# Optimization experiments

Measured on AMD Instinct MI355X. Metric: run time of the kernel, lower is better.

Reference implementation:

```python
import jax, jax.numpy as jnp
import numpy as np

NUM_EXPERTS = 8
TOP_K = 2
HIDDEN = 512
INTER = 2048
BALANCE_COEF = 0.01


def setup_inputs() -> dict:
    key = jax.random.key(0)
    ks = jax.random.split(key, 5)
    B, S = 2, 1024
    scale_in = 1.0 / np.sqrt(HIDDEN)
    scale_mid = 1.0 / np.sqrt(INTER)
    return {
        "hidden_states": jax.random.normal(ks[0], (B, S, HIDDEN), jnp.float32),
        "w_router": jax.random.normal(ks[1], (HIDDEN, NUM_EXPERTS), jnp.float32) * scale_in,
        "b_router": jnp.zeros((NUM_EXPERTS,), jnp.float32),
        "w1": jax.random.normal(ks[2], (NUM_EXPERTS, HIDDEN, INTER), jnp.float32) * scale_in,
        "b1": jnp.zeros((NUM_EXPERTS, INTER), jnp.float32),
        "w2": jax.random.normal(ks[3], (NUM_EXPERTS, INTER, HIDDEN), jnp.float32) * scale_mid,
        "b2": jnp.zeros((NUM_EXPERTS, HIDDEN), jnp.float32),
    }


def reference(hidden_states, w_router, b_router, w1, b1, w2, b2):
    B, S, H = hidden_states.shape
    E, K = NUM_EXPERTS, TOP_K

    # ---- Router: softmax over experts, top-k selection, renormalized weights ----
    logits = jnp.einsum("bsh,he->bse", hidden_states, w_router) + b_router  # (B,S,E)
    probs = jax.nn.softmax(logits, axis=-1)
    top_vals, top_idx = jax.lax.top_k(probs, K)                              # (B,S,K)
    routing_weights = top_vals / jnp.sum(top_vals, axis=-1, keepdims=True)   # renorm to sum 1

    # ---- Load-balancing auxiliary loss: coef * E * sum_e f_e * P_e ----
    assign = jax.nn.one_hot(top_idx, E, dtype=probs.dtype)                   # (B,S,K,E)
    f = jnp.mean(assign, axis=(0, 1, 2))                                     # fraction routed per expert
    P = jnp.mean(probs, axis=(0, 1))                                         # mean router prob per expert
    balance_loss = BALANCE_COEF * E * jnp.sum(f * P)

    # ---- Phase 1: flatten (B,S,H) -> (B*S*K, H) token-slots ----
    T = B * S * K
    tokens_flat = jnp.broadcast_to(hidden_states[:, :, None, :], (B, S, K, H)).reshape(T, H)
    weights_flat = routing_weights.reshape(T)
    experts_flat = top_idx.reshape(T)

    # ---- Phase 2: per-expert MLP, masked combine ----
    out_flat = jnp.zeros_like(tokens_flat)
    for e in range(E):
        hmid = jax.nn.gelu(tokens_flat @ w1[e] + b1[e])                      # (T, INTER)
        y = hmid @ w2[e] + b2[e]                                             # (T, H)
        mask = (experts_flat == e)
        out_flat = out_flat + jnp.where(mask[:, None], y * weights_flat[:, None], 0.0)

    # ---- Phase 3: combine over K and residual ----
    combined = out_flat.reshape(B, S, K, H).sum(axis=2)
    output = combined + hidden_states
    return output, balance_loss
```

## Files before the change

kernel.cpp:

```cpp
#include <hip/hip_runtime.h>
#include <math.h>

#define NT 2048
#define TSLOTS 4096
#define HID 512
#define INTER 2048
#define NE 8
#define TM 128
#define BK 32
#define MAXTILES 40
#define PSLOTS 5120

#define WS_HMID      0
#define WS_PROBS     0
#define WS_TOPIDX    65536
#define WS_TOPW      81920
#define WS_TILE_E    20971520
#define WS_TILE_B    20971776
#define WS_TILE_V    20972032
#define WS_PERM      20972288
#define WS_PW        20992768
#define WS_ISLOT     21013248
#define WS_XB        21029632
#define WS_WT        23126784
#define WS_Y         39904000

typedef __attribute__((ext_vector_type(8))) short bf16x8;
typedef __attribute__((ext_vector_type(4))) float f32x4;
typedef __attribute__((ext_vector_type(8))) unsigned short ushort8;

__device__ __forceinline__ unsigned short f2bf(float f) {
    union { float f; unsigned u; } v; v.f = f;
    unsigned r = v.u + 0x7FFF + ((v.u >> 16) & 1);
    return (unsigned short)(r >> 16);
}
__device__ __forceinline__ float bf2f(unsigned short b) {
    union { unsigned u; float f; } v; v.u = ((unsigned)b) << 16;
    return v.f;
}

__device__ __forceinline__ void gload16(const void* g, void* l) {
    __builtin_amdgcn_global_load_lds(
        (const __attribute__((address_space(1))) unsigned int*)g,
        (__attribute__((address_space(3))) unsigned int*)l, 16, 0, 0);
}

__device__ __forceinline__ float gelu_tanh(float x) {
    float x3 = x * x * x;
    return 0.5f * x * (1.0f + tanhf(0.7978845608028654f * (x + 0.044715f * x3)));
}

__global__ __launch_bounds__(64) void route_k(
    const float* __restrict__ hs, const float* __restrict__ wr,
    const float* __restrict__ br,
    unsigned short* __restrict__ xb,
    float* __restrict__ probs, int* __restrict__ topidx, float* __restrict__ topw)
{
    int t = blockIdx.x;
    int lane = threadIdx.x;
    const float* x = hs + (size_t)t * HID + lane * 8;
    float4 v0 = *(const float4*)x;
    float4 v1 = *(const float4*)(x + 4);

    ushort8 ob;
    ob[0] = f2bf(v0.x); ob[1] = f2bf(v0.y); ob[2] = f2bf(v0.z); ob[3] = f2bf(v0.w);
    ob[4] = f2bf(v1.x); ob[5] = f2bf(v1.y); ob[6] = f2bf(v1.z); ob[7] = f2bf(v1.w);
    *(ushort8*)(xb + (size_t)t * HID + lane * 8) = ob;

    float xv[8] = {v0.x, v0.y, v0.z, v0.w, v1.x, v1.y, v1.z, v1.w};
    float acc[NE];
#pragma unroll
    for (int e = 0; e < NE; e++) acc[e] = 0.0f;
    const float* w = wr + (size_t)lane * 8 * NE;
#pragma unroll
    for (int j = 0; j < 8; j++) {
        float4 wa = *(const float4*)(w + j * NE);
        float4 wb = *(const float4*)(w + j * NE + 4);
        acc[0] += xv[j] * wa.x; acc[1] += xv[j] * wa.y;
        acc[2] += xv[j] * wa.z; acc[3] += xv[j] * wa.w;
        acc[4] += xv[j] * wb.x; acc[5] += xv[j] * wb.y;
        acc[6] += xv[j] * wb.z; acc[7] += xv[j] * wb.w;
    }
#pragma unroll
    for (int off = 32; off > 0; off >>= 1) {
#pragma unroll
        for (int e = 0; e < NE; e++) acc[e] += __shfl_down(acc[e], off);
    }
    if (lane == 0) {
        float l[NE], p[NE];
        float m = -1e30f;
#pragma unroll
        for (int e = 0; e < NE; e++) { l[e] = acc[e] + br[e]; m = fmaxf(m, l[e]); }
        float s = 0.0f;
#pragma unroll
        for (int e = 0; e < NE; e++) { p[e] = expf(l[e] - m); s += p[e]; }
        float inv = 1.0f / s;
#pragma unroll
        for (int e = 0; e < NE; e++) { p[e] *= inv; probs[(size_t)t * NE + e] = p[e]; }
        int i1 = 0;
#pragma unroll
        for (int e = 1; e < NE; e++) if (p[e] > p[i1]) i1 = e;
        int i2 = (i1 == 0) ? 1 : 0;
#pragma unroll
        for (int e = 0; e < NE; e++) if (e != i1 && p[e] > p[i2]) i2 = e;
        float denom = 1.0f / (p[i1] + p[i2]);
        topidx[2 * t]     = i1;
        topidx[2 * t + 1] = i2;
        topw[2 * t]       = p[i1] * denom;
        topw[2 * t + 1]   = p[i2] * denom;
    }
}

__global__ __launch_bounds__(256) void plan_k(
    const float* __restrict__ probs, const int* __restrict__ topidx,
    const float* __restrict__ topw,
    int* __restrict__ tile_e, int* __restrict__ tile_b, int* __restrict__ tile_v,
    int* __restrict__ perm, float* __restrict__ pw, int* __restrict__ islot,
    float* __restrict__ loss_out)
{
    int tid = threadIdx.x;
    int lane = tid & 63, wave = tid >> 6;

    float ps[NE];
    int c[NE];
#pragma unroll
    for (int e = 0; e < NE; e++) { ps[e] = 0.0f; c[e] = 0; }
    for (int t = tid; t < NT; t += 256) {
        float4 p0 = *(const float4*)&probs[(size_t)t * NE];
        float4 p1 = *(const float4*)&probs[(size_t)t * NE + 4];
        ps[0] += p0.x; ps[1] += p0.y; ps[2] += p0.z; ps[3] += p0.w;
        ps[4] += p1.x; ps[5] += p1.y; ps[6] += p1.z; ps[7] += p1.w;
    }
    for (int t = tid; t < TSLOTS; t += 256) c[topidx[t]]++;
#pragma unroll
    for (int off = 32; off > 0; off >>= 1) {
#pragma unroll
        for (int e = 0; e < NE; e++) {
            ps[e] += __shfl_down(ps[e], off);
            c[e]  += __shfl_down(c[e], off);
        }
    }
    __shared__ float sps[4][NE];
    __shared__ int sc[4][NE];
    __shared__ int scur[NE];
    if (lane == 0) {
#pragma unroll
        for (int e = 0; e < NE; e++) { sps[wave][e] = ps[e]; sc[wave][e] = c[e]; }
    }
    __syncthreads();
    if (tid == 0) {
        float loss = 0.0f;
        int b = 0, tidx = 0;
        for (int e = 0; e < NE; e++) {
            float pse = sps[0][e] + sps[1][e] + sps[2][e] + sps[3][e];
            int ce = sc[0][e] + sc[1][e] + sc[2][e] + sc[3][e];
            loss += ((float)ce / (float)TSLOTS) * (pse / (float)NT);
            int nt = (ce + TM - 1) / TM;
            scur[e] = b;
            for (int i = 0; i < nt; i++) {
                tile_e[tidx] = e;
                tile_b[tidx] = b + i * TM;
                int v = ce - i * TM;
                tile_v[tidx] = v > TM ? TM : v;
                tidx++;
            }
            b += nt * TM;
        }
        for (; tidx < MAXTILES; tidx++) tile_e[tidx] = -1;
        loss_out[0] = 0.01f * (float)NE * loss;
    }
    __syncthreads();
    for (int t = tid; t < TSLOTS; t += 256) {
        int e = topidx[t];
        int p = atomicAdd(&scur[e], 1);
        perm[p] = t;
        pw[p] = topw[t];
        islot[t] = p;
    }
}

__global__ __launch_bounds__(256) void convT_k(const float* __restrict__ src,
                                               unsigned short* __restrict__ dst,
                                               int K, int N)
{
    int e = blockIdx.z;
    int n0 = blockIdx.x * 32, k0 = blockIdx.y * 32;
    const float* s = src + (size_t)e * K * N;
    unsigned short* d = dst + (size_t)e * N * K;
    __shared__ float T[32][33];
    int tid = threadIdx.x;
    int r = tid >> 3, c4 = (tid & 7) * 4;
    float4 v = *(const float4*)(s + (size_t)(k0 + r) * N + n0 + c4);
    T[r][c4 + 0] = v.x; T[r][c4 + 1] = v.y; T[r][c4 + 2] = v.z; T[r][c4 + 3] = v.w;
    __syncthreads();
    ushort4 o;
    o.x = f2bf(T[c4 + 0][r]); o.y = f2bf(T[c4 + 1][r]);
    o.z = f2bf(T[c4 + 2][r]); o.w = f2bf(T[c4 + 3][r]);
    *(ushort4*)(d + (size_t)(n0 + r) * K + k0 + c4) = o;
}

__global__ __launch_bounds__(256) void gemm1_k(
    const unsigned short* __restrict__ xb, const unsigned short* __restrict__ w1t,
    const float* __restrict__ b1,
    const int* __restrict__ tile_e, const int* __restrict__ tile_b,
    const int* __restrict__ tile_v, const int* __restrict__ perm,
    unsigned short* __restrict__ hmid)
{
    int tt = blockIdx.y;
    int e = tile_e[tt];
    if (e < 0) return;
    int p0 = tile_b[tt], nv = tile_v[tt];
    int n0 = blockIdx.x * 128;

    __shared__ unsigned short As[128 * BK];
    __shared__ unsigned short Bs[128 * BK];

    int tid = threadIdx.x;
    int lane = tid & 63, wave = tid >> 6;
    int wm = (wave >> 1) * 64, wn = (wave & 1) * 64;

    int r1 = tid >> 2, r2 = 64 + r1;
    int kseg = (tid & 3) * 8;
    int tok1 = perm[p0 + ((r1 < nv) ? r1 : 0)] >> 1;
    int tok2 = perm[p0 + ((r2 < nv) ? r2 : 0)] >> 1;
    const unsigned short* a1p = xb + (size_t)tok1 * HID + kseg;
    const unsigned short* a2p = xb + (size_t)tok2 * HID + kseg;
    const unsigned short* bbase = w1t + (size_t)e * INTER * HID;
    const unsigned short* b1p = bbase + (size_t)(n0 + r1) * HID + kseg;
    const unsigned short* b2p = bbase + (size_t)(n0 + r2) * HID + kseg;

    f32x4 acc[4][4] = {};
    int fm = lane & 15, fq = lane >> 4;

    for (int k0 = 0; k0 < HID; k0 += BK) {
        __syncthreads();
        gload16(a1p + k0, (void*)(As + tid * 8));
        gload16(a2p + k0, (void*)(As + 2048 + tid * 8));
        gload16(b1p + k0, (void*)(Bs + tid * 8));
        gload16(b2p + k0, (void*)(Bs + 2048 + tid * 8));
        __syncthreads();
        bf16x8 af[4], bfr[4];
#pragma unroll
        for (int t = 0; t < 4; t++)
            af[t] = *(const bf16x8*)&As[(wm + t * 16 + fm) * BK + fq * 8];
#pragma unroll
        for (int t = 0; t < 4; t++)
            bfr[t] = *(const bf16x8*)&Bs[(wn + t * 16 + fm) * BK + fq * 8];
#pragma unroll
        for (int mt = 0; mt < 4; mt++)
#pragma unroll
            for (int nt = 0; nt < 4; nt++)
                acc[mt][nt] = __builtin_amdgcn_mfma_f32_16x16x32_bf16(
                    af[mt], bfr[nt], acc[mt][nt], 0, 0, 0);
    }

    int cn = lane & 15, crb = (lane >> 4) * 4;
#pragma unroll
    for (int mt = 0; mt < 4; mt++) {
#pragma unroll
        for (int r = 0; r < 4; r++) {
            int m = wm + mt * 16 + crb + r;
            size_t rowoff = (size_t)(p0 + m) * INTER;
#pragma unroll
            for (int nt = 0; nt < 4; nt++) {
                int gn = n0 + wn + nt * 16 + cn;
                float vv = acc[mt][nt][r] + b1[e * INTER + gn];
                hmid[rowoff + gn] = f2bf(gelu_tanh(vv));
            }
        }
    }
}

__global__ __launch_bounds__(256) void gemm2_k(
    const unsigned short* __restrict__ hmid, const unsigned short* __restrict__ w2t,
    const float* __restrict__ b2,
    const int* __restrict__ tile_e, const int* __restrict__ tile_b,
    unsigned short* __restrict__ y)
{
    int tt = blockIdx.y;
    int e = tile_e[tt];
    if (e < 0) return;
    int p0 = tile_b[tt];
    int n0 = blockIdx.x * 64;
    int kz = blockIdx.z;
    int kbeg = kz * (INTER / 2), kend = kbeg + INTER / 2;
    unsigned short* yk = y + (size_t)kz * PSLOTS * HID;

    __shared__ unsigned short As[128 * BK];
    __shared__ unsigned short Bs[64 * BK];

    int tid = threadIdx.x;
    int lane = tid & 63, wave = tid >> 6;
    int wm = (wave >> 1) * 64, wn = (wave & 1) * 32;

    int r1 = tid >> 2, r2 = 64 + r1;
    int kseg = (tid & 3) * 8;
    const unsigned short* a1p = hmid + (size_t)(p0 + r1) * INTER + kseg;
    const unsigned short* a2p = hmid + (size_t)(p0 + r2) * INTER + kseg;
    const unsigned short* bbase = w2t + (size_t)e * HID * INTER;
    const unsigned short* bp = bbase + (size_t)(n0 + r1) * INTER + kseg;

    f32x4 acc[4][2] = {};
    int fm = lane & 15, fq = lane >> 4;

    for (int k0 = kbeg; k0 < kend; k0 += BK) {
        __syncthreads();
        gload16(a1p + k0, (void*)(As + tid * 8));
        gload16(a2p + k0, (void*)(As + 2048 + tid * 8));
        gload16(bp + k0, (void*)(Bs + tid * 8));
        __syncthreads();
        bf16x8 af[4], bfr[2];
#pragma unroll
        for (int t = 0; t < 4; t++)
            af[t] = *(const bf16x8*)&As[(wm + t * 16 + fm) * BK + fq * 8];
#pragma unroll
        for (int t = 0; t < 2; t++)
            bfr[t] = *(const bf16x8*)&Bs[(wn + t * 16 + fm) * BK + fq * 8];
#pragma unroll
        for (int mt = 0; mt < 4; mt++)
#pragma unroll
            for (int nt = 0; nt < 2; nt++)
                acc[mt][nt] = __builtin_amdgcn_mfma_f32_16x16x32_bf16(
                    af[mt], bfr[nt], acc[mt][nt], 0, 0, 0);
    }

    int cn = lane & 15, crb = (lane >> 4) * 4;
#pragma unroll
    for (int mt = 0; mt < 4; mt++) {
#pragma unroll
        for (int r = 0; r < 4; r++) {
            int m = wm + mt * 16 + crb + r;
            size_t rowoff = (size_t)(p0 + m) * HID;
#pragma unroll
            for (int nt = 0; nt < 2; nt++) {
                int gn = n0 + wn + nt * 16 + cn;
                float bias = (kz == 0) ? b2[e * HID + gn] : 0.0f;
                yk[rowoff + gn] = f2bf(acc[mt][nt][r] + bias);
            }
        }
    }
}

__global__ __launch_bounds__(64) void combine_k(
    const float* __restrict__ hs, const unsigned short* __restrict__ y,
    const int* __restrict__ islot, const float* __restrict__ pw,
    float* __restrict__ out)
{
    int t = blockIdx.x;
    int lane = threadIdx.x;
    int pA = islot[2 * t], pB = islot[2 * t + 1];
    float wA = pw[pA], wB = pw[pB];
    int c = lane * 8;
    const unsigned short* yA0 = y + (size_t)pA * HID + c;
    const unsigned short* yB0 = y + (size_t)pB * HID + c;
    const unsigned short* yA1 = yA0 + (size_t)PSLOTS * HID;
    const unsigned short* yB1 = yB0 + (size_t)PSLOTS * HID;
    ushort8 a0 = *(const ushort8*)yA0;
    ushort8 a1 = *(const ushort8*)yA1;
    ushort8 b0 = *(const ushort8*)yB0;
    ushort8 b1 = *(const ushort8*)yB1;
    const float* h = hs + (size_t)t * HID + c;
    float4 h0 = *(const float4*)h;
    float4 h1 = *(const float4*)(h + 4);
    float o[8];
#pragma unroll
    for (int j = 0; j < 8; j++)
        o[j] = wA * (bf2f(a0[j]) + bf2f(a1[j])) + wB * (bf2f(b0[j]) + bf2f(b1[j]));
    float4 r0 = {o[0] + h0.x, o[1] + h0.y, o[2] + h0.z, o[3] + h0.w};
    float4 r1 = {o[4] + h1.x, o[5] + h1.y, o[6] + h1.z, o[7] + h1.w};
    float* op = out + (size_t)t * HID + c;
    *(float4*)op = r0;
    *(float4*)(op + 4) = r1;
}

extern "C" void kernel_launch(void* const* d_in, const int* in_sizes, int n_in,
                              void* d_out, int out_size, void* d_ws, size_t ws_size,
                              hipStream_t stream) {
    const float* hs = (const float*)d_in[0];
    const float* wr = (const float*)d_in[1];
    const float* br = (const float*)d_in[2];
    const float* w1 = (const float*)d_in[3];
    const float* b1 = (const float*)d_in[4];
    const float* w2 = (const float*)d_in[5];
    const float* b2 = (const float*)d_in[6];
    float* out = (float*)d_out;

    char* ws = (char*)d_ws;
    float* probs           = (float*)(ws + WS_PROBS);
    int*   topidx          = (int*)(ws + WS_TOPIDX);
    float* topw            = (float*)(ws + WS_TOPW);
    int*   tile_e          = (int*)(ws + WS_TILE_E);
    int*   tile_b          = (int*)(ws + WS_TILE_B);
    int*   tile_v          = (int*)(ws + WS_TILE_V);
    int*   perm            = (int*)(ws + WS_PERM);
    float* pw              = (float*)(ws + WS_PW);
    int*   islot           = (int*)(ws + WS_ISLOT);
    unsigned short* xb     = (unsigned short*)(ws + WS_XB);
    unsigned short* wt     = (unsigned short*)(ws + WS_WT);
    unsigned short* hmid   = (unsigned short*)(ws + WS_HMID);
    unsigned short* y      = (unsigned short*)(ws + WS_Y);

    route_k<<<NT, 64, 0, stream>>>(hs, wr, br, xb, probs, topidx, topw);
    plan_k<<<1, 256, 0, stream>>>(probs, topidx, topw, tile_e, tile_b, tile_v,
                                  perm, pw, islot, out + (size_t)NT * HID);
    convT_k<<<dim3(INTER / 32, HID / 32, NE), 256, 0, stream>>>(w1, wt, HID, INTER);
    gemm1_k<<<dim3(INTER / 128, MAXTILES), 256, 0, stream>>>(
        xb, wt, b1, tile_e, tile_b, tile_v, perm, hmid);
    convT_k<<<dim3(HID / 32, INTER / 32, NE), 256, 0, stream>>>(w2, wt, INTER, HID);
    gemm2_k<<<dim3(HID / 64, MAXTILES, 2), 256, 0, stream>>>(
        hmid, wt, b2, tile_e, tile_b, y);
    combine_k<<<NT, 64, 0, stream>>>(hs, y, islot, pw, out);
}
```

Before: 211.7 us.

## Shrink expert row tiles to 64, widen K step with XOR-swizzled LDS, faster GELU

Both expert GEMMs now use 64-row token tiles instead of 128, which cuts padding waste per expert and raises the tile count and block parallelism. The K step doubles to 64, and LDS rows are XOR-swizzled to avoid bank conflicts on fragment reads. The tanh GELU is replaced by the equivalent sigmoid form using __expf. Smaller M tiles reduce the MFMA work per loaded B tile, so weight traffic rises, and the workspace offsets are recomputed for the new slot counts.

```diff
diff --git a/kernel.cpp b/kernel.cpp
--- a/kernel.cpp
+++ b/kernel.cpp
@@ -6,24 +6,24 @@
 #define HID 512
 #define INTER 2048
 #define NE 8
-#define TM 128
-#define BK 32
-#define MAXTILES 40
-#define PSLOTS 5120
+#define TM 64
+#define BKG 64
+#define MAXTILES 72
+#define PSLOTS 4608
 
 #define WS_HMID      0
 #define WS_PROBS     0
 #define WS_TOPIDX    65536
 #define WS_TOPW      81920
-#define WS_TILE_E    20971520
-#define WS_TILE_B    20971776
-#define WS_TILE_V    20972032
-#define WS_PERM      20972288
-#define WS_PW        20992768
-#define WS_ISLOT     21013248
-#define WS_XB        21029632
-#define WS_WT        23126784
-#define WS_Y         39904000
+#define WS_TILE_E    18874368
+#define WS_TILE_B    18874880
+#define WS_TILE_V    18875392
+#define WS_PERM      18875904
+#define WS_PW        18894336
+#define WS_ISLOT     18912768
+#define WS_XB        18929152
+#define WS_WT        21026304
+#define WS_Y         37803520
 
 typedef __attribute__((ext_vector_type(8))) short bf16x8;
 typedef __attribute__((ext_vector_type(4))) float f32x4;
@@ -45,9 +45,9 @@
         (__attribute__((address_space(3))) unsigned int*)l, 16, 0, 0);
 }
 
-__device__ __forceinline__ float gelu_tanh(float x) {
-    float x3 = x * x * x;
-    return 0.5f * x * (1.0f + tanhf(0.7978845608028654f * (x + 0.044715f * x3)));
+__device__ __forceinline__ float gelu_fast(float x) {
+    float t = 1.5957691f * x + 0.0713548f * x * x * x;
+    return x / (1.0f + __expf(-t));
 }
 
 __global__ __launch_bounds__(64) void route_k(
@@ -212,51 +212,64 @@
     int p0 = tile_b[tt], nv = tile_v[tt];
     int n0 = blockIdx.x * 128;
 
-    __shared__ unsigned short As[128 * BK];
-    __shared__ unsigned short Bs[128 * BK];
+    __shared__ unsigned short As[64 * 64];
+    __shared__ unsigned short Bs[128 * 64];
 
     int tid = threadIdx.x;
     int lane = tid & 63, wave = tid >> 6;
-    int wm = (wave >> 1) * 64, wn = (wave & 1) * 64;
-
-    int r1 = tid >> 2, r2 = 64 + r1;
-    int kseg = (tid & 3) * 8;
-    int tok1 = perm[p0 + ((r1 < nv) ? r1 : 0)] >> 1;
-    int tok2 = perm[p0 + ((r2 < nv) ? r2 : 0)] >> 1;
-    const unsigned short* a1p = xb + (size_t)tok1 * HID + kseg;
-    const unsigned short* a2p = xb + (size_t)tok2 * HID + kseg;
+    int wm = (wave >> 1) * 32, wn = (wave & 1) * 64;
+
+    int rA = tid >> 3, gs = tid & 7;
+    int rA2 = rA + 32;
+    int tokA = perm[p0 + ((rA < nv) ? rA : 0)] >> 1;
+    int tokA2 = perm[p0 + ((rA2 < nv) ? rA2 : 0)] >> 1;
+    const unsigned short* apt1 = xb + (size_t)tokA * HID + (gs ^ (rA & 7)) * 8;
+    const unsigned short* apt2 = xb + (size_t)tokA2 * HID + (gs ^ (rA2 & 7)) * 8;
     const unsigned short* bbase = w1t + (size_t)e * INTER * HID;
-    const unsigned short* b1p = bbase + (size_t)(n0 + r1) * HID + kseg;
-    const unsigned short* b2p = bbase + (size_t)(n0 + r2) * HID + kseg;
-
-    f32x4 acc[4][4] = {};
+    const unsigned short* bpt0 = bbase + (size_t)(n0 + rA) * HID + (gs ^ (rA & 7)) * 8;
+    const unsigned short* bpt1 = bbase + (size_t)(n0 + rA + 32) * HID + (gs ^ ((rA + 32) & 7)) * 8;
+    const unsigned short* bpt2 = bbase + (size_t)(n0 + rA + 64) * HID + (gs ^ ((rA + 64) & 7)) * 8;
+    const unsigned short* bpt3 = bbase + (size_t)(n0 + rA + 96) * HID + (gs ^ ((rA + 96) & 7)) * 8;
+
+    f32x4 acc[2][4] = {};
     int fm = lane & 15, fq = lane >> 4;
 
-    for (int k0 = 0; k0 < HID; k0 += BK) {
+    for (int k0 = 0; k0 < HID; k0 += BKG) {
         __syncthreads();
-        gload16(a1p + k0, (void*)(As + tid * 8));
-        gload16(a2p + k0, (void*)(As + 2048 + tid * 8));
-        gload16(b1p + k0, (void*)(Bs + tid * 8));
-        gload16(b2p + k0, (void*)(Bs + 2048 + tid * 8));
+        gload16(apt1 + k0, (void*)(As + tid * 8));
+        gload16(apt2 + k0, (void*)(As + 2048 + tid * 8));
+        gload16(bpt0 + k0, (void*)(Bs + tid * 8));
+        gload16(bpt1 + k0, (void*)(Bs + 2048 + tid * 8));
+        gload16(bpt2 + k0, (void*)(Bs + 4096 + tid * 8));
+        gload16(bpt3 + k0, (void*)(Bs + 6144 + tid * 8));
         __syncthreads();
-        bf16x8 af[4], bfr[4];
-#pragma unroll
-        for (int t = 0; t < 4; t++)
-            af[t] = *(const bf16x8*)&As[(wm + t * 16 + fm) * BK + fq * 8];
-#pragma unroll
-        for (int t = 0; t < 4; t++)
-            bfr[t] = *(const bf16x8*)&Bs[(wn + t * 16 + fm) * BK + fq * 8];
-#pragma unroll
-        for (int mt = 0; mt < 4; mt++)
-#pragma unroll
-            for (int nt = 0; nt < 4; nt++)
-                acc[mt][nt] = __builtin_amdgcn_mfma_f32_16x16x32_bf16(
-                    af[mt], bfr[nt], acc[mt][nt], 0, 0, 0);
+#pragma unroll
+        for (int kk = 0; kk < 2; kk++) {
+            bf16x8 af[2], bfr[4];
+#pragma unroll
+            for (int mt = 0; mt < 2; mt++) {
+                int R = wm + mt * 16 + fm;
+                int G = (kk * 4 + fq) ^ (R & 7);
+                af[mt] = *(const bf16x8*)&As[R * 64 + G * 8];
+            }
+#pragma unroll
+            for (int nt = 0; nt < 4; nt++) {
+                int R = wn + nt * 16 + fm;
+                int G = (kk * 4 + fq) ^ (R & 7);
+                bfr[nt] = *(const bf16x8*)&Bs[R * 64 + G * 8];
+            }
+#pragma unroll
+            for (int mt = 0; mt < 2; mt++)
+#pragma unroll
+                for (int nt = 0; nt < 4; nt++)
+                    acc[mt][nt] = __builtin_amdgcn_mfma_f32_16x16x32_bf16(
+                        af[mt], bfr[nt], acc[mt][nt], 0, 0, 0);
+        }
     }
 
     int cn = lane & 15, crb = (lane >> 4) * 4;
 #pragma unroll
-    for (int mt = 0; mt < 4; mt++) {
+    for (int mt = 0; mt < 2; mt++) {
 #pragma unroll
         for (int r = 0; r < 4; r++) {
             int m = wm + mt * 16 + crb + r;
@@ -265,7 +278,7 @@
             for (int nt = 0; nt < 4; nt++) {
                 int gn = n0 + wn + nt * 16 + cn;
                 float vv = acc[mt][nt][r] + b1[e * INTER + gn];
-                hmid[rowoff + gn] = f2bf(gelu_tanh(vv));
+                hmid[rowoff + gn] = f2bf(gelu_fast(vv));
             }
         }
     }
@@ -286,47 +299,58 @@
     int kbeg = kz * (INTER / 2), kend = kbeg + INTER / 2;
     unsigned short* yk = y + (size_t)kz * PSLOTS * HID;
 
-    __shared__ unsigned short As[128 * BK];
-    __shared__ unsigned short Bs[64 * BK];
+    __shared__ unsigned short As[64 * 64];
+    __shared__ unsigned short Bs[64 * 64];
 
     int tid = threadIdx.x;
     int lane = tid & 63, wave = tid >> 6;
-    int wm = (wave >> 1) * 64, wn = (wave & 1) * 32;
-
-    int r1 = tid >> 2, r2 = 64 + r1;
-    int kseg = (tid & 3) * 8;
-    const unsigned short* a1p = hmid + (size_t)(p0 + r1) * INTER + kseg;
-    const unsigned short* a2p = hmid + (size_t)(p0 + r2) * INTER + kseg;
+    int wm = (wave >> 1) * 32, wn = (wave & 1) * 32;
+
+    int rA = tid >> 3, gs = tid & 7;
+    int rA2 = rA + 32;
+    const unsigned short* apt1 = hmid + (size_t)(p0 + rA) * INTER + (gs ^ (rA & 7)) * 8;
+    const unsigned short* apt2 = hmid + (size_t)(p0 + rA2) * INTER + (gs ^ (rA2 & 7)) * 8;
     const unsigned short* bbase = w2t + (size_t)e * HID * INTER;
-    const unsigned short* bp = bbase + (size_t)(n0 + r1) * INTER + kseg;
-
-    f32x4 acc[4][2] = {};
+    const unsigned short* bpt1 = bbase + (size_t)(n0 + rA) * INTER + (gs ^ (rA & 7)) * 8;
+    const unsigned short* bpt2 = bbase + (size_t)(n0 + rA2) * INTER + (gs ^ (rA2 & 7)) * 8;
+
+    f32x4 acc[2][2] = {};
     int fm = lane & 15, fq = lane >> 4;
 
-    for (int k0 = kbeg; k0 < kend; k0 += BK) {
+    for (int k0 = kbeg; k0 < kend; k0 += BKG) {
         __syncthreads();
-        gload16(a1p + k0, (void*)(As + tid * 8));
-        gload16(a2p + k0, (void*)(As + 2048 + tid * 8));
-        gload16(bp + k0, (void*)(Bs + tid * 8));
+        gload16(apt1 + k0, (void*)(As + tid * 8));
+        gload16(apt2 + k0, (void*)(As + 2048 + tid * 8));
+        gload16(bpt1 + k0, (void*)(Bs + tid * 8));
+        gload16(bpt2 + k0, (void*)(Bs + 2048 + tid * 8));
         __syncthreads();
-        bf16x8 af[4], bfr[2];
-#pragma unroll
-        for (int t = 0; t < 4; t++)
-            af[t] = *(const bf16x8*)&As[(wm + t * 16 + fm) * BK + fq * 8];
-#pragma unroll
-        for (int t = 0; t < 2; t++)
-            bfr[t] = *(const bf16x8*)&Bs[(wn + t * 16 + fm) * BK + fq * 8];
-#pragma unroll
-        for (int mt = 0; mt < 4; mt++)
-#pragma unroll
-            for (int nt = 0; nt < 2; nt++)
-                acc[mt][nt] = __builtin_amdgcn_mfma_f32_16x16x32_bf16(
-                    af[mt], bfr[nt], acc[mt][nt], 0, 0, 0);
+#pragma unroll
+        for (int kk = 0; kk < 2; kk++) {
+            bf16x8 af[2], bfr[2];
+#pragma unroll
+            for (int mt = 0; mt < 2; mt++) {
+                int R = wm + mt * 16 + fm;
+                int G = (kk * 4 + fq) ^ (R & 7);
+                af[mt] = *(const bf16x8*)&As[R * 64 + G * 8];
+            }
+#pragma unroll
+            for (int nt = 0; nt < 2; nt++) {
+                int R = wn + nt * 16 + fm;
+                int G = (kk * 4 + fq) ^ (R & 7);
+                bfr[nt] = *(const bf16x8*)&Bs[R * 64 + G * 8];
+            }
+#pragma unroll
+            for (int mt = 0; mt < 2; mt++)
+#pragma unroll
+                for (int nt = 0; nt < 2; nt++)
+                    acc[mt][nt] = __builtin_amdgcn_mfma_f32_16x16x32_bf16(
+                        af[mt], bfr[nt], acc[mt][nt], 0, 0, 0);
+        }
     }
 
     int cn = lane & 15, crb = (lane >> 4) * 4;
 #pragma unroll
-    for (int mt = 0; mt < 4; mt++) {
+    for (int mt = 0; mt < 2; mt++) {
 #pragma unroll
         for (int r = 0; r < 4; r++) {
             int m = wm + mt * 16 + crb + r;
```

New measurement: 193.0 us. -8.8%, faster.
